# Optimization experiments

Hardware: AMD Instinct MI355X
Metric: run time of the kernel (lower is better)

Reference implementation:

```python
import jax, jax.numpy as jnp
import numpy as np

HID = 768        # config.hidden_size
MM_HID = 1024    # config.mmodal_hidden_size
N_Q = 64         # config.num_queries
WIN = 512        # config.window_size
LN_EPS = 1e-5


def _window_starts(m, n, w):
    # mirrors split_tensor's start-index logic (static, computed in numpy)
    step = max(1, (m - w) // (n - 1))
    starts = []
    for i in range(n):
        s = i * step
        if s + w > m:
            s = m - w
        starts.append(s)
    return np.asarray(starts, dtype=np.int32)


def layernorm(x, g, b):
    mu = jnp.mean(x, axis=-1, keepdims=True)
    var = jnp.var(x, axis=-1, keepdims=True)
    return (x - mu) * jax.lax.rsqrt(var + LN_EPS) * g + b


def setup_inputs() -> dict:
    key = jax.random.key(0)
    ks = jax.random.split(key, 12)
    b, m, li = 4, 8192, 77
    s = lambda fan_in: 1.0 / np.sqrt(fan_in)
    inp = {
        'x_mmodal': jax.random.normal(ks[0], (b, m, MM_HID), jnp.float32),
        'inst_feats': jax.random.normal(ks[1], (b, li, HID), jnp.float32),
        'queries': jax.random.normal(ks[2], (1, N_Q, HID), jnp.float32),
        'W_proj': jax.random.normal(ks[3], (HID, HID), jnp.float32) * s(HID),
        'b_proj': jnp.zeros((HID,), jnp.float32),
        'W_kv_inst': jax.random.normal(ks[4], (HID, 2 * HID), jnp.float32) * s(HID),
        'b_kv_inst': jnp.zeros((2 * HID,), jnp.float32),
        'W_out_inst': jax.random.normal(ks[5], (HID, HID), jnp.float32) * s(HID),
        'b_out_inst': jnp.zeros((HID,), jnp.float32),
        'W_kv_mm': jax.random.normal(ks[6], (MM_HID, 2 * HID), jnp.float32) * s(MM_HID),
        'b_kv_mm': jnp.zeros((2 * HID,), jnp.float32),
        'W_out_mm': jax.random.normal(ks[7], (HID, HID), jnp.float32) * s(HID),
        'b_out_mm': jnp.zeros((HID,), jnp.float32),
        'ln_g': jnp.ones((HID,), jnp.float32),
        'ln_b': jnp.zeros((HID,), jnp.float32),
    }
    return inp


def reference(x_mmodal, inst_feats, queries, W_proj, b_proj, W_kv_inst,
              b_kv_inst, W_out_inst, b_out_inst, W_kv_mm, b_kv_mm,
              W_out_mm, b_out_mm, ln_g, ln_b):
    b = x_mmodal.shape[0]
    scale = 1.0 / jnp.sqrt(jnp.asarray(HID, x_mmodal.dtype))

    # ---- dense cross-attention over instruction features ----
    inst = inst_feats @ W_proj + b_proj                      # (b, li, d)
    k, v = jnp.split(inst @ W_kv_inst + b_kv_inst, 2, axis=-1)
    k = layernorm(k, ln_g, ln_b)
    v = layernorm(v, ln_g, ln_b)
    q = jnp.broadcast_to(queries, (b, N_Q, HID))
    attn = jnp.einsum('bnd,bmd->bnm', q, k) * scale
    attn = jax.nn.softmax(attn, axis=-1)
    q = jnp.einsum('bnm,bmd->bnd', attn, v)
    q = layernorm(q @ W_out_inst + b_out_inst, ln_g, ln_b)

    # ---- swin-style overlapping windowed cross-attention over mmodal ----
    k, v = jnp.split(x_mmodal @ W_kv_mm + b_kv_mm, 2, axis=-1)
    k = layernorm(k, ln_g, ln_b)
    v = layernorm(v, ln_g, ln_b)
    m = k.shape[1]
    starts = _window_starts(m, N_Q, WIN)                     # (n,)
    idx = jnp.asarray(starts[:, None] + np.arange(WIN))      # (n, w)
    kw = k[:, idx]                                           # (b, n, w, d)
    vw = v[:, idx]                                           # (b, n, w, d)
    a = jnp.einsum('bnd,bnwd->bnw', q, kw) * scale
    a = jax.nn.softmax(a, axis=-1)
    out = jnp.einsum('bnw,bnwd->bnd', a, vw)
    out = layernorm(out @ W_out_mm + b_out_mm, ln_g, ln_b)
    return out
```

## Files before the change

### kernel.cpp

```cpp
#include <hip/hip_runtime.h>

#define HIDDEN 768
#define NQ 64
#define WINSZ 512
#define MSEQ 8192
#define BATCH 4
#define LI 77
#define MMHID 1024
#define LN_EPS 1e-5f
#define SCALE_QK 0.03608439182435161f

typedef __attribute__((ext_vector_type(8))) short short8v;
typedef __attribute__((ext_vector_type(4))) float f32x4;
typedef __attribute__((ext_vector_type(8))) unsigned short u16x8;

#define AS1 __attribute__((address_space(1)))
#define AS3 __attribute__((address_space(3)))

__device__ inline unsigned short f2bf(float f) {
    unsigned u = __float_as_uint(f);
    u += 0x7fffu + ((u >> 16) & 1u);
    return (unsigned short)(u >> 16);
}
__device__ inline float bf2f(unsigned short h) {
    return __uint_as_float(((unsigned)h) << 16);
}

__device__ inline void block_reduce2_256(float& s1, float& s2, float* sm) {
    #pragma unroll
    for (int o = 32; o; o >>= 1) { s1 += __shfl_down(s1, o); s2 += __shfl_down(s2, o); }
    int lane = threadIdx.x & 63, w = threadIdx.x >> 6;
    __syncthreads();
    if (lane == 0) { sm[w] = s1; sm[4 + w] = s2; }
    __syncthreads();
    s1 = sm[0] + sm[1] + sm[2] + sm[3];
    s2 = sm[4] + sm[5] + sm[6] + sm[7];
}

__global__ __launch_bounds__(256) void cvt_kernel(const float* __restrict__ in,
                                                  unsigned short* __restrict__ out, int n8) {
    int i = blockIdx.x * 256 + threadIdx.x;
    if (i >= n8) return;
    const float4* p = (const float4*)(in + (size_t)i * 8);
    float4 a = p[0], b = p[1];
    u16x8 o;
    o[0] = f2bf(a.x); o[1] = f2bf(a.y); o[2] = f2bf(a.z); o[3] = f2bf(a.w);
    o[4] = f2bf(b.x); o[5] = f2bf(b.y); o[6] = f2bf(b.z); o[7] = f2bf(b.w);
    *(u16x8*)(out + (size_t)i * 8) = o;
}

__global__ __launch_bounds__(256) void cvt_pad_kernel(const float* __restrict__ in,
                                                      unsigned short* __restrict__ out,
                                                      int n8_valid, int n8_total) {
    int i = blockIdx.x * 256 + threadIdx.x;
    if (i >= n8_total) return;
    u16x8 o = {};
    if (i < n8_valid) {
        const float4* p = (const float4*)(in + (size_t)i * 8);
        float4 a = p[0], b = p[1];
        o[0] = f2bf(a.x); o[1] = f2bf(a.y); o[2] = f2bf(a.z); o[3] = f2bf(a.w);
        o[4] = f2bf(b.x); o[5] = f2bf(b.y); o[6] = f2bf(b.z); o[7] = f2bf(b.w);
    }
    *(u16x8*)(out + (size_t)i * 8) = o;
}

__global__ __launch_bounds__(256) void cvt_q_pad_kernel(const float* __restrict__ q2,
                                                        unsigned short* __restrict__ q2bf) {
    int i = blockIdx.x * 256 + threadIdx.x;
    if (i >= BATCH * 128 * HIDDEN) return;
    int b = i / (128 * HIDDEN);
    int rem = i - b * 128 * HIDDEN;
    int r = rem / HIDDEN, d = rem - r * HIDDEN;
    float v = 0.f;
    if (r < 64) v = q2[((size_t)(b * 64 + r)) * HIDDEN + d] * SCALE_QK;
    q2bf[i] = f2bf(v);
}

__global__ __launch_bounds__(256) void transW_kernel(const float* __restrict__ W,
                                                     unsigned short* __restrict__ Wt,
                                                     int D, int C) {
    __shared__ float tile[32][33];
    int n0 = blockIdx.x * 32, k0 = blockIdx.y * 32;
    int tx = threadIdx.x, ty = threadIdx.y;
    #pragma unroll
    for (int i = 0; i < 32; i += 8)
        tile[ty + i][tx] = W[(size_t)(k0 + ty + i) * C + n0 + tx];
    __syncthreads();
    #pragma unroll
    for (int i = 0; i < 32; i += 8)
        Wt[(size_t)(n0 + ty + i) * D + k0 + tx] = f2bf(tile[tx][ty + i]);
}

#define GM 32768
#define GN 1536
#define GK 1024

__global__ __launch_bounds__(256) void gemm_kv_kernel(const unsigned short* __restrict__ A,
                                                      const unsigned short* __restrict__ Bt,
                                                      const float* __restrict__ bias,
                                                      unsigned short* __restrict__ C) {
    __shared__ unsigned short sA[128 * 64];
    __shared__ unsigned short sB[128 * 64];

    int nwg = gridDim.x;
    int bid = blockIdx.x;
    int wg = bid;
    if ((nwg & 7) == 0) { int cpx = nwg >> 3; wg = (bid & 7) * cpx + (bid >> 3); }
    int bm = wg / (GN / 128), bn = wg % (GN / 128);
    int row0 = bm * 128, col0 = bn * 128;

    int tid = threadIdx.x;
    int lane = tid & 63, wid = tid >> 6;
    int wr = wid >> 1, wc = wid & 1;

    f32x4 acc[4][4] = {};

    int rS[4], cS[4];
    #pragma unroll
    for (int i = 0; i < 4; i++) {
        int ch = wid * 4 + i;
        int r = ch * 8 + (lane >> 3);
        rS[i] = r;
        cS[i] = ((lane & 7) ^ (r & 7)) << 3;
    }

    for (int k0 = 0; k0 < GK; k0 += 64) {
        #pragma unroll
        for (int i = 0; i < 4; i++) {
            int ch = wid * 4 + i;
            const unsigned short* ga = A + (size_t)(row0 + rS[i]) * GK + k0 + cS[i];
            __builtin_amdgcn_global_load_lds((const AS1 unsigned int*)ga,
                                             (AS3 unsigned int*)&sA[ch * 512], 16, 0, 0);
            const unsigned short* gb = Bt + (size_t)(col0 + rS[i]) * GK + k0 + cS[i];
            __builtin_amdgcn_global_load_lds((const AS1 unsigned int*)gb,
                                             (AS3 unsigned int*)&sB[ch * 512], 16, 0, 0);
        }
        __syncthreads();

        #pragma unroll
        for (int kk = 0; kk < 64; kk += 32) {
            int ko = (kk + ((lane >> 4) << 3)) * 2;
            short8v af[4], bf[4];
            #pragma unroll
            for (int m = 0; m < 4; m++) {
                int r = wr * 64 + m * 16 + (lane & 15);
                int addr = r * 128 + (ko ^ ((r & 7) << 4));
                af[m] = *(const short8v*)((const char*)sA + addr);
            }
            #pragma unroll
            for (int n = 0; n < 4; n++) {
                int r = wc * 64 + n * 16 + (lane & 15);
                int addr = r * 128 + (ko ^ ((r & 7) << 4));
                bf[n] = *(const short8v*)((const char*)sB + addr);
            }
            #pragma unroll
            for (int m = 0; m < 4; m++)
                #pragma unroll
                for (int n = 0; n < 4; n++)
                    acc[m][n] = __builtin_amdgcn_mfma_f32_16x16x32_bf16(af[m], bf[n], acc[m][n], 0, 0, 0);
        }
        __syncthreads();
    }

    int crow = (lane >> 4) * 4;
    int ccol = lane & 15;
    #pragma unroll
    for (int m = 0; m < 4; m++) {
        #pragma unroll
        for (int n = 0; n < 4; n++) {
            int gc = col0 + wc * 64 + n * 16 + ccol;
            float bv = bias[gc];
            #pragma unroll
            for (int j = 0; j < 4; j++) {
                int gr = row0 + wr * 64 + m * 16 + crow + j;
                C[(size_t)gr * GN + gc] = f2bf(acc[m][n][j] + bv);
            }
        }
    }
}

template <int TK, bool OUT_BF16>
__global__ __launch_bounds__(256) void gemm_tile_kernel(const unsigned short* __restrict__ A,
                                                        const unsigned short* __restrict__ Bt,
                                                        const float* __restrict__ bias,
                                                        void* __restrict__ Cout, int N) {
    __shared__ unsigned short sA[128 * 64];
    __shared__ unsigned short sB[128 * 64];

    int row0 = blockIdx.x * 128, col0 = blockIdx.y * 128;
    int tid = threadIdx.x;
    int lane = tid & 63, wid = tid >> 6;
    int wr = wid >> 1, wc = wid & 1;

    f32x4 acc[4][4] = {};

    int rS[4], cS[4];
    #pragma unroll
    for (int i = 0; i < 4; i++) {
        int ch = wid * 4 + i;
        int r = ch * 8 + (lane >> 3);
        rS[i] = r;
        cS[i] = ((lane & 7) ^ (r & 7)) << 3;
    }

    for (int k0 = 0; k0 < TK; k0 += 64) {
        #pragma unroll
        for (int i = 0; i < 4; i++) {
            int ch = wid * 4 + i;
            const unsigned short* ga = A + (size_t)(row0 + rS[i]) * TK + k0 + cS[i];
            __builtin_amdgcn_global_load_lds((const AS1 unsigned int*)ga,
                                             (AS3 unsigned int*)&sA[ch * 512], 16, 0, 0);
            const unsigned short* gb = Bt + (size_t)(col0 + rS[i]) * TK + k0 + cS[i];
            __builtin_amdgcn_global_load_lds((const AS1 unsigned int*)gb,
                                             (AS3 unsigned int*)&sB[ch * 512], 16, 0, 0);
        }
        __syncthreads();

        #pragma unroll
        for (int kk = 0; kk < 64; kk += 32) {
            int ko = (kk + ((lane >> 4) << 3)) * 2;
            short8v af[4], bf[4];
            #pragma unroll
            for (int m = 0; m < 4; m++) {
                int r = wr * 64 + m * 16 + (lane & 15);
                int addr = r * 128 + (ko ^ ((r & 7) << 4));
                af[m] = *(const short8v*)((const char*)sA + addr);
            }
            #pragma unroll
            for (int n = 0; n < 4; n++) {
                int r = wc * 64 + n * 16 + (lane & 15);
                int addr = r * 128 + (ko ^ ((r & 7) << 4));
                bf[n] = *(const short8v*)((const char*)sB + addr);
            }
            #pragma unroll
            for (int m = 0; m < 4; m++)
                #pragma unroll
                for (int n = 0; n < 4; n++)
                    acc[m][n] = __builtin_amdgcn_mfma_f32_16x16x32_bf16(af[m], bf[n], acc[m][n], 0, 0, 0);
        }
        __syncthreads();
    }

    int crow = (lane >> 4) * 4;
    int ccol = lane & 15;
    #pragma unroll
    for (int m = 0; m < 4; m++) {
        #pragma unroll
        for (int n = 0; n < 4; n++) {
            int gc = col0 + wc * 64 + n * 16 + ccol;
            float bv = bias[gc];
            #pragma unroll
            for (int j = 0; j < 4; j++) {
                int gr = row0 + wr * 64 + m * 16 + crow + j;
                float v = acc[m][n][j] + bv;
                if (OUT_BF16) ((unsigned short*)Cout)[(size_t)gr * N + gc] = f2bf(v);
                else          ((float*)Cout)[(size_t)gr * N + gc] = v;
            }
        }
    }
}

__global__ __launch_bounds__(256) void gemm_scores_kernel(const unsigned short* __restrict__ Aall,
                                                          const unsigned short* __restrict__ kv,
                                                          float* __restrict__ scores) {
    __shared__ unsigned short sA[128 * 64];
    __shared__ unsigned short sB[128 * 64];

    int b = blockIdx.y;
    int col0 = blockIdx.x * 128;
    const unsigned short* A = Aall + (size_t)b * 128 * HIDDEN;
    const unsigned short* Bt = kv + (size_t)b * MSEQ * 1536;

    int tid = threadIdx.x;
    int lane = tid & 63, wid = tid >> 6;
    int wr = wid >> 1, wc = wid & 1;

    f32x4 acc[4][4] = {};

    int rS[4], cS[4];
    #pragma unroll
    for (int i = 0; i < 4; i++) {
        int ch = wid * 4 + i;
        int r = ch * 8 + (lane >> 3);
        rS[i] = r;
        cS[i] = ((lane & 7) ^ (r & 7)) << 3;
    }

    for (int k0 = 0; k0 < HIDDEN; k0 += 64) {
        #pragma unroll
        for (int i = 0; i < 4; i++) {
            int ch = wid * 4 + i;
            const unsigned short* ga = A + (size_t)rS[i] * HIDDEN + k0 + cS[i];
            __builtin_amdgcn_global_load_lds((const AS1 unsigned int*)ga,
                                             (AS3 unsigned int*)&sA[ch * 512], 16, 0, 0);
            const unsigned short* gb = Bt + (size_t)(col0 + rS[i]) * 1536 + k0 + cS[i];
            __builtin_amdgcn_global_load_lds((const AS1 unsigned int*)gb,
                                             (AS3 unsigned int*)&sB[ch * 512], 16, 0, 0);
        }
        __syncthreads();

        #pragma unroll
        for (int kk = 0; kk < 64; kk += 32) {
            int ko = (kk + ((lane >> 4) << 3)) * 2;
            short8v af[4], bf[4];
            #pragma unroll
            for (int m = 0; m < 4; m++) {
                int r = wr * 64 + m * 16 + (lane & 15);
                int addr = r * 128 + (ko ^ ((r & 7) << 4));
                af[m] = *(const short8v*)((const char*)sA + addr);
            }
            #pragma unroll
            for (int n = 0; n < 4; n++) {
                int r = wc * 64 + n * 16 + (lane & 15);
                int addr = r * 128 + (ko ^ ((r & 7) << 4));
                bf[n] = *(const short8v*)((const char*)sB + addr);
            }
            #pragma unroll
            for (int m = 0; m < 4; m++)
                #pragma unroll
                for (int n = 0; n < 4; n++)
                    acc[m][n] = __builtin_amdgcn_mfma_f32_16x16x32_bf16(af[m], bf[n], acc[m][n], 0, 0, 0);
        }
        __syncthreads();
    }

    int crow = (lane >> 4) * 4;
    int ccol = lane & 15;
    #pragma unroll
    for (int m = 0; m < 4; m++) {
        #pragma unroll
        for (int n = 0; n < 4; n++) {
            int gc = col0 + wc * 64 + n * 16 + ccol;
            #pragma unroll
            for (int j = 0; j < 4; j++) {
                int gr = wr * 64 + m * 16 + crow + j;
                if (gr < 64)
                    scores[((size_t)(b * 64 + gr)) * MSEQ + gc] = acc[m][n][j];
            }
        }
    }
}

__global__ __launch_bounds__(512) void win_softmax_kernel(const float* __restrict__ scores,
                                                          unsigned short* __restrict__ P_abs) {
    int bidx = blockIdx.x;
    int b = bidx >> 6, n = bidx & 63;
    int step = (MSEQ - WINSZ) / (NQ - 1);
    int s = n * step;
    if (s + WINSZ > MSEQ) s = MSEQ - WINSZ;

    __shared__ float sm[8];
    int t = threadIdx.x, lane = t & 63, w = t >> 6;
    const float* srow = scores + ((size_t)(b * 64 + n)) * MSEQ;
    float a = srow[s + t];

    float m = a;
    #pragma unroll
    for (int o = 32; o; o >>= 1) m = fmaxf(m, __shfl_down(m, o));
    if (lane == 0) sm[w] = m;
    __syncthreads();
    m = sm[0];
    #pragma unroll
    for (int i = 1; i < 8; i++) m = fmaxf(m, sm[i]);
    float e = expf(a - m);
    float ssum = e;
    #pragma unroll
    for (int o = 32; o; o >>= 1) ssum += __shfl_down(ssum, o);
    __syncthreads();
    if (lane == 0) sm[w] = ssum;
    __syncthreads();
    ssum = 0;
    #pragma unroll
    for (int i = 0; i < 8; i++) ssum += sm[i];

    unsigned short* prow = P_abs + ((size_t)(b * 64 + n)) * MSEQ;
    for (int pos = t; pos < MSEQ; pos += 512)
        if (pos < s || pos >= s + WINSZ) prow[pos] = 0;
    prow[s + t] = f2bf(e / ssum);
}

__global__ __launch_bounds__(768) void pv_chunk_kernel(const unsigned short* __restrict__ P_abs,
                                                       const unsigned short* __restrict__ kv,
                                                       float* __restrict__ out_acc) {
    int b = blockIdx.y;
    int r0 = blockIdx.x * 64;
    int t = threadIdx.x;

    int n_lo = (r0 >= 512) ? ((r0 - 512) / 121 + 1) : 0;
    int n_hi = (r0 + 63) / 121;
    if (n_hi > 63) n_hi = 63;

    __shared__ float pw[5][64];
    if (t < 5 * 64) {
        int ni = t >> 6, r = t & 63;
        int n = n_lo + ni;
        float v = 0.f;
        if (n <= n_hi)
            v = bf2f(P_abs[((size_t)(b * 64 + n)) * MSEQ + r0 + r]);
        pw[ni][r] = v;
    }
    __syncthreads();

    const unsigned short* vbase = kv + ((size_t)(b * MSEQ + r0)) * 1536 + 768;
    float acc[5] = {};
    #pragma unroll 8
    for (int r = 0; r < 64; ++r) {
        float v = bf2f(vbase[(size_t)r * 1536 + t]);
        #pragma unroll
        for (int ni = 0; ni < 5; ni++) acc[ni] = fmaf(v, pw[ni][r], acc[ni]);
    }
    #pragma unroll
    for (int ni = 0; ni < 5; ni++) {
        int n = n_lo + ni;
        if (n <= n_hi)
            atomicAdd(&out_acc[((size_t)(b * 64 + n)) * HIDDEN + t], acc[ni]);
    }
}

__global__ __launch_bounds__(256) void ln_bf16_kernel(unsigned short* __restrict__ kv,
                                                      const float* __restrict__ g,
                                                      const float* __restrict__ b) {
    int rh = blockIdx.x;
    unsigned short* p = kv + (size_t)rh * 768;
    int t = threadIdx.x;
    float x0 = bf2f(p[t]), x1 = bf2f(p[t + 256]), x2 = bf2f(p[t + 512]);
    float s = x0 + x1 + x2, s2 = x0 * x0 + x1 * x1 + x2 * x2;
    __shared__ float sm[8];
    block_reduce2_256(s, s2, sm);
    float mu = s * (1.f / 768.f);
    float var = s2 * (1.f / 768.f) - mu * mu;
    float inv = rsqrtf(var + LN_EPS);
    p[t]       = f2bf((x0 - mu) * inv * g[t]       + b[t]);
    p[t + 256] = f2bf((x1 - mu) * inv * g[t + 256] + b[t + 256]);
    p[t + 512] = f2bf((x2 - mu) * inv * g[t + 512] + b[t + 512]);
}

__global__ __launch_bounds__(256) void ln_f32_rows(float* __restrict__ base,
                                                   const float* __restrict__ g,
                                                   const float* __restrict__ b) {
    int rh = blockIdx.x;
    float* p = base + (size_t)rh * 768;
    int t = threadIdx.x;
    float x0 = p[t], x1 = p[t + 256], x2 = p[t + 512];
    float s = x0 + x1 + x2, s2 = x0 * x0 + x1 * x1 + x2 * x2;
    __shared__ float sm[8];
    block_reduce2_256(s, s2, sm);
    float mu = s * (1.f / 768.f);
    float var = s2 * (1.f / 768.f) - mu * mu;
    float inv = rsqrtf(var + LN_EPS);
    p[t]       = (x0 - mu) * inv * g[t]       + b[t];
    p[t + 256] = (x1 - mu) * inv * g[t + 256] + b[t + 256];
    p[t + 512] = (x2 - mu) * inv * g[t + 512] + b[t + 512];
}

__global__ __launch_bounds__(256) void attn_inst_kernel(const float* __restrict__ queries,
                                                        const float* __restrict__ kv,
                                                        unsigned short* __restrict__ qatt) {
    int bidx = blockIdx.x;
    int b = bidx >> 6, n = bidx & 63;
    __shared__ float qs[HIDDEN];
    __shared__ float sc[LI], sc2[LI];
    int t = threadIdx.x, lane = t & 63, w = t >> 6;
    const float* q = queries + (size_t)n * HIDDEN;
    for (int d = t; d < HIDDEN; d += 256) qs[d] = q[d];
    __syncthreads();
    const float* kb = kv + (size_t)b * LI * 1536;
    for (int j = w; j < LI; j += 4) {
        const float* kr = kb + (size_t)j * 1536;
        float a = 0;
        #pragma unroll
        for (int i = 0; i < 12; i++) { int d = lane + i * 64; a = fmaf(kr[d], qs[d], a); }
        #pragma unroll
        for (int o = 32; o; o >>= 1) a += __shfl_down(a, o);
        if (lane == 0) sc[j] = a * SCALE_QK;
    }
    __syncthreads();
    float m = -1e30f;
    for (int j = 0; j < LI; j++) m = fmaxf(m, sc[j]);
    if (t < LI) sc2[t] = expf(sc[t] - m);
    __syncthreads();
    float s = 0;
    for (int j = 0; j < LI; j++) s += sc2[j];
    float inv = 1.f / s;
    float o0 = 0, o1 = 0, o2 = 0;
    for (int j = 0; j < LI; j++) {
        float p = sc2[j] * inv;
        const float* vr = kb + (size_t)j * 1536 + 768;
        o0 = fmaf(p, vr[t], o0);
        o1 = fmaf(p, vr[t + 256], o1);
        o2 = fmaf(p, vr[t + 512], o2);
    }
    unsigned short* orow = qatt + ((size_t)b * NQ + n) * HIDDEN;
    orow[t] = f2bf(o0); orow[t + 256] = f2bf(o1); orow[t + 512] = f2bf(o2);
}

extern "C" void kernel_launch(void* const* d_in, const int* in_sizes, int n_in,
                              void* d_out, int out_size, void* d_ws, size_t ws_size,
                              hipStream_t stream) {
    (void)in_sizes; (void)n_in; (void)out_size; (void)ws_size;
    const float* x_mm    = (const float*)d_in[0];
    const float* instf   = (const float*)d_in[1];
    const float* queries = (const float*)d_in[2];
    const float* W_proj  = (const float*)d_in[3];
    const float* b_proj  = (const float*)d_in[4];
    const float* W_kvi   = (const float*)d_in[5];
    const float* b_kvi   = (const float*)d_in[6];
    const float* W_oi    = (const float*)d_in[7];
    const float* b_oi    = (const float*)d_in[8];
    const float* W_kvm   = (const float*)d_in[9];
    const float* b_kvm   = (const float*)d_in[10];
    const float* W_om    = (const float*)d_in[11];
    const float* b_om    = (const float*)d_in[12];
    const float* ln_g    = (const float*)d_in[13];
    const float* ln_b    = (const float*)d_in[14];
    float* out = (float*)d_out;

    char* ws = (char*)d_ws;
    size_t off = 0;
    auto carve = [&](size_t bytes) -> char* {
        char* p = ws + off;
        off += (bytes + 255) & ~(size_t)255;
        return p;
    };
    unsigned short* x_bf   = (unsigned short*)carve((size_t)BATCH * MSEQ * MMHID * 2);
    unsigned short* wtm_bf = (unsigned short*)carve((size_t)2 * HIDDEN * MMHID * 2);
    unsigned short* kv_mm  = (unsigned short*)carve((size_t)BATCH * MSEQ * 2 * HIDDEN * 2);
    unsigned short* wp_bf  = (unsigned short*)carve((size_t)768 * 768 * 2);
    unsigned short* wkvi_bf= (unsigned short*)carve((size_t)1536 * 768 * 2);
    unsigned short* woi_bf = (unsigned short*)carve((size_t)768 * 768 * 2);
    unsigned short* wom_bf = (unsigned short*)carve((size_t)768 * 768 * 2);
    unsigned short* a1_bf  = (unsigned short*)carve((size_t)384 * 768 * 2);
    unsigned short* inst_bf= (unsigned short*)carve((size_t)384 * 768 * 2);
    float*          kv_inst= (float*)carve((size_t)384 * 1536 * 4);
    unsigned short* qatt_bf= (unsigned short*)carve((size_t)256 * 768 * 2);
    float*          q2     = (float*)carve((size_t)256 * 768 * 4);
    unsigned short* q2bf   = (unsigned short*)carve((size_t)BATCH * 128 * 768 * 2);
    float*          scores = (float*)carve((size_t)BATCH * 64 * MSEQ * 4);
    unsigned short* P_abs  = (unsigned short*)carve((size_t)BATCH * 64 * MSEQ * 2);
    float*          o_acc  = (float*)carve((size_t)BATCH * 64 * 768 * 4);
    unsigned short* a_bf   = (unsigned short*)carve((size_t)256 * 768 * 2);

    transW_kernel<<<dim3(1536 / 32, 1024 / 32), dim3(32, 8), 0, stream>>>(W_kvm, wtm_bf, 1024, 1536);
    transW_kernel<<<dim3(768 / 32, 768 / 32), dim3(32, 8), 0, stream>>>(W_proj, wp_bf, 768, 768);
    transW_kernel<<<dim3(1536 / 32, 768 / 32), dim3(32, 8), 0, stream>>>(W_kvi, wkvi_bf, 768, 1536);
    transW_kernel<<<dim3(768 / 32, 768 / 32), dim3(32, 8), 0, stream>>>(W_oi, woi_bf, 768, 768);
    transW_kernel<<<dim3(768 / 32, 768 / 32), dim3(32, 8), 0, stream>>>(W_om, wom_bf, 768, 768);

    int n8 = BATCH * MSEQ * MMHID / 8;
    cvt_kernel<<<(n8 + 255) / 256, 256, 0, stream>>>(x_mm, x_bf, n8);
    gemm_kv_kernel<<<(GM / 128) * (GN / 128), 256, 0, stream>>>(x_bf, wtm_bf, b_kvm, kv_mm);
    ln_bf16_kernel<<<BATCH * MSEQ * 2, 256, 0, stream>>>(kv_mm, ln_g, ln_b);

    cvt_pad_kernel<<<(384 * 768 / 8 + 255) / 256, 256, 0, stream>>>(instf, a1_bf,
                                                                    BATCH * LI * 768 / 8, 384 * 768 / 8);
    gemm_tile_kernel<768, true><<<dim3(3, 6), 256, 0, stream>>>(a1_bf, wp_bf, b_proj, inst_bf, 768);
    gemm_tile_kernel<768, false><<<dim3(3, 12), 256, 0, stream>>>(inst_bf, wkvi_bf, b_kvi, kv_inst, 1536);
    ln_f32_rows<<<BATCH * LI * 2, 256, 0, stream>>>(kv_inst, ln_g, ln_b);
    attn_inst_kernel<<<BATCH * NQ, 256, 0, stream>>>(queries, kv_inst, qatt_bf);
    gemm_tile_kernel<768, false><<<dim3(2, 6), 256, 0, stream>>>(qatt_bf, woi_bf, b_oi, q2, 768);
    ln_f32_rows<<<BATCH * NQ, 256, 0, stream>>>(q2, ln_g, ln_b);

    hipMemsetAsync(o_acc, 0, (size_t)BATCH * 64 * 768 * 4, stream);
    cvt_q_pad_kernel<<<(BATCH * 128 * 768 + 255) / 256, 256, 0, stream>>>(q2, q2bf);
    gemm_scores_kernel<<<dim3(MSEQ / 128, BATCH), 256, 0, stream>>>(q2bf, kv_mm, scores);
    win_softmax_kernel<<<BATCH * NQ, 512, 0, stream>>>(scores, P_abs);
    pv_chunk_kernel<<<dim3(MSEQ / 64, BATCH), 768, 0, stream>>>(P_abs, kv_mm, o_acc);
    cvt_kernel<<<(256 * 768 / 8 + 255) / 256, 256, 0, stream>>>(o_acc, a_bf, 256 * 768 / 8);

    gemm_tile_kernel<768, false><<<dim3(2, 6), 256, 0, stream>>>(a_bf, wom_bf, b_om, out, 768);
    ln_f32_rows<<<BATCH * NQ, 256, 0, stream>>>(out, ln_g, ln_b);
}
```

Before: 367.6 us.

## Fold mmodal K/V layernorm into scores and output instead of rewriting KV

The in-place layernorm pass over the large bf16 KV buffer is replaced by a read-only stats kernel that stores per-row mu*inv and inv. The normalization is folded in algebraically in three places. The query is pre-scaled by gamma, and the scores are corrected with inv and a mean term built from the sum of the scaled query. The probabilities are scaled by the V-row inv, and the output applies gamma and beta after subtracting a weighted mean term. This removes a full write of the KV buffer. Separately, the five weight-transpose launches are merged into one batched launch. The cost is extra small kernels and reductions, plus some numerical sensitivity from working on un-normalized bf16 values.

Result: faster. 350.2 us (-4.7%).

```diff
diff --git a/kernel.cpp b/kernel.cpp
--- a/kernel.cpp
+++ b/kernel.cpp
@@ -64,24 +64,44 @@
     *(u16x8*)(out + (size_t)i * 8) = o;
 }
 
-__global__ __launch_bounds__(256) void cvt_q_pad_kernel(const float* __restrict__ q2,
-                                                        unsigned short* __restrict__ q2bf) {
-    int i = blockIdx.x * 256 + threadIdx.x;
-    if (i >= BATCH * 128 * HIDDEN) return;
-    int b = i / (128 * HIDDEN);
-    int rem = i - b * 128 * HIDDEN;
-    int r = rem / HIDDEN, d = rem - r * HIDDEN;
-    float v = 0.f;
-    if (r < 64) v = q2[((size_t)(b * 64 + r)) * HIDDEN + d] * SCALE_QK;
-    q2bf[i] = f2bf(v);
-}
-
-__global__ __launch_bounds__(256) void transW_kernel(const float* __restrict__ W,
-                                                     unsigned short* __restrict__ Wt,
-                                                     int D, int C) {
+__global__ __launch_bounds__(256) void cvt_q_kernel(const float* __restrict__ q2,
+                                                    const float* __restrict__ g,
+                                                    unsigned short* __restrict__ q2bf,
+                                                    float* __restrict__ qgsum) {
+    int blk = blockIdx.x;
+    int b = blk >> 7, r = blk & 127;
+    int t = threadIdx.x;
+    unsigned short* orow = q2bf + (size_t)blk * HIDDEN;
+    if (r >= 64) {
+        orow[t] = 0; orow[t + 256] = 0; orow[t + 512] = 0;
+        return;
+    }
+    const float* qrow = q2 + ((size_t)(b * 64 + r)) * HIDDEN;
+    float v0 = qrow[t]       * g[t]       * SCALE_QK;
+    float v1 = qrow[t + 256] * g[t + 256] * SCALE_QK;
+    float v2 = qrow[t + 512] * g[t + 512] * SCALE_QK;
+    orow[t] = f2bf(v0); orow[t + 256] = f2bf(v1); orow[t + 512] = f2bf(v2);
+    float s = v0 + v1 + v2, s2 = 0.f;
+    __shared__ float sm[8];
+    block_reduce2_256(s, s2, sm);
+    if (t == 0) qgsum[b * 64 + r] = s;
+}
+
+struct TWJobs {
+    const float* W[5];
+    unsigned short* Wt[5];
+    int D[5];
+    int C[5];
+};
+__global__ __launch_bounds__(256) void transW_all_kernel(TWJobs tw) {
+    int z = blockIdx.z;
+    int C = tw.C[z], D = tw.D[z];
+    int n0 = blockIdx.x * 32, k0 = blockIdx.y * 32;
+    if (n0 >= C || k0 >= D) return;
+    const float* W = tw.W[z];
+    unsigned short* Wt = tw.Wt[z];
     __shared__ float tile[32][33];
-    int n0 = blockIdx.x * 32, k0 = blockIdx.y * 32;
-    int tx = threadIdx.x, ty = threadIdx.y;
+    int tx = threadIdx.x & 31, ty = (threadIdx.x >> 5);
     #pragma unroll
     for (int i = 0; i < 32; i += 8)
         tile[ty + i][tx] = W[(size_t)(k0 + ty + i) * C + n0 + tx];
@@ -179,6 +199,23 @@
     }
 }
 
+__global__ __launch_bounds__(256) void stats_kernel(const unsigned short* __restrict__ kv,
+                                                    float2* __restrict__ stats) {
+    int rh = blockIdx.x;
+    const unsigned short* p = kv + (size_t)rh * 768;
+    int t = threadIdx.x;
+    float x0 = bf2f(p[t]), x1 = bf2f(p[t + 256]), x2 = bf2f(p[t + 512]);
+    float s = x0 + x1 + x2, s2 = x0 * x0 + x1 * x1 + x2 * x2;
+    __shared__ float sm[8];
+    block_reduce2_256(s, s2, sm);
+    if (t == 0) {
+        float mu = s * (1.f / 768.f);
+        float var = s2 * (1.f / 768.f) - mu * mu;
+        float inv = rsqrtf(var + LN_EPS);
+        stats[rh] = make_float2(mu * inv, inv);
+    }
+}
+
 template <int TK, bool OUT_BF16>
 __global__ __launch_bounds__(256) void gemm_tile_kernel(const unsigned short* __restrict__ A,
                                                         const unsigned short* __restrict__ Bt,
@@ -342,7 +379,10 @@
 }
 
 __global__ __launch_bounds__(512) void win_softmax_kernel(const float* __restrict__ scores,
-                                                          unsigned short* __restrict__ P_abs) {
+                                                          const float2* __restrict__ stats,
+                                                          const float* __restrict__ qgsum,
+                                                          unsigned short* __restrict__ P_abs,
+                                                          float* __restrict__ s2out) {
     int bidx = blockIdx.x;
     int b = bidx >> 6, n = bidx & 63;
     int step = (MSEQ - WINSZ) / (NQ - 1);
@@ -351,8 +391,11 @@
 
     __shared__ float sm[8];
     int t = threadIdx.x, lane = t & 63, w = t >> 6;
-    const float* srow = scores + ((size_t)(b * 64 + n)) * MSEQ;
-    float a = srow[s + t];
+    int r_abs = s + t;
+    size_t rowidx = (size_t)b * MSEQ + r_abs;
+    float2 stk = stats[rowidx * 2 + 0];
+    float qg = qgsum[b * 64 + n];
+    float a = stk.y * scores[((size_t)(b * 64 + n)) * MSEQ + r_abs] - qg * stk.x;
 
     float m = a;
     #pragma unroll
@@ -372,11 +415,27 @@
     ssum = 0;
     #pragma unroll
     for (int i = 0; i < 8; i++) ssum += sm[i];
+    float p = e / ssum;
+
+    float2 stv = stats[rowidx * 2 + 1];
+    float pt = p * stv.y;
+    float s2p = p * stv.x;
+    #pragma unroll
+    for (int o = 32; o; o >>= 1) s2p += __shfl_down(s2p, o);
+    __syncthreads();
+    if (lane == 0) sm[w] = s2p;
+    __syncthreads();
+    if (t == 0) {
+        float s2 = 0;
+        #pragma unroll
+        for (int i = 0; i < 8; i++) s2 += sm[i];
+        s2out[b * 64 + n] = s2;
+    }
 
     unsigned short* prow = P_abs + ((size_t)(b * 64 + n)) * MSEQ;
     for (int pos = t; pos < MSEQ; pos += 512)
         if (pos < s || pos >= s + WINSZ) prow[pos] = 0;
-    prow[s + t] = f2bf(e / ssum);
+    prow[r_abs] = f2bf(pt);
 }
 
 __global__ __launch_bounds__(768) void pv_chunk_kernel(const unsigned short* __restrict__ P_abs,
@@ -417,22 +476,15 @@
     }
 }
 
-__global__ __launch_bounds__(256) void ln_bf16_kernel(unsigned short* __restrict__ kv,
-                                                      const float* __restrict__ g,
-                                                      const float* __restrict__ b) {
-    int rh = blockIdx.x;
-    unsigned short* p = kv + (size_t)rh * 768;
-    int t = threadIdx.x;
-    float x0 = bf2f(p[t]), x1 = bf2f(p[t + 256]), x2 = bf2f(p[t + 512]);
-    float s = x0 + x1 + x2, s2 = x0 * x0 + x1 * x1 + x2 * x2;
-    __shared__ float sm[8];
-    block_reduce2_256(s, s2, sm);
-    float mu = s * (1.f / 768.f);
-    float var = s2 * (1.f / 768.f) - mu * mu;
-    float inv = rsqrtf(var + LN_EPS);
-    p[t]       = f2bf((x0 - mu) * inv * g[t]       + b[t]);
-    p[t + 256] = f2bf((x1 - mu) * inv * g[t + 256] + b[t + 256]);
-    p[t + 512] = f2bf((x2 - mu) * inv * g[t + 512] + b[t + 512]);
+__global__ __launch_bounds__(256) void out_affine_kernel(const float* __restrict__ o_acc,
+                                                         const float* __restrict__ s2,
+                                                         const float* __restrict__ g,
+                                                         const float* __restrict__ bb,
+                                                         unsigned short* __restrict__ a_bf) {
+    int i = blockIdx.x * 256 + threadIdx.x;
+    if (i >= BATCH * NQ * HIDDEN) return;
+    int n = i / HIDDEN, d = i - n * HIDDEN;
+    a_bf[i] = f2bf(g[d] * (o_acc[i] - s2[n]) + bb[d]);
 }
 
 __global__ __launch_bounds__(256) void ln_f32_rows(float* __restrict__ base,
@@ -539,17 +591,22 @@
     unsigned short* P_abs  = (unsigned short*)carve((size_t)BATCH * 64 * MSEQ * 2);
     float*          o_acc  = (float*)carve((size_t)BATCH * 64 * 768 * 4);
     unsigned short* a_bf   = (unsigned short*)carve((size_t)256 * 768 * 2);
-
-    transW_kernel<<<dim3(1536 / 32, 1024 / 32), dim3(32, 8), 0, stream>>>(W_kvm, wtm_bf, 1024, 1536);
-    transW_kernel<<<dim3(768 / 32, 768 / 32), dim3(32, 8), 0, stream>>>(W_proj, wp_bf, 768, 768);
-    transW_kernel<<<dim3(1536 / 32, 768 / 32), dim3(32, 8), 0, stream>>>(W_kvi, wkvi_bf, 768, 1536);
-    transW_kernel<<<dim3(768 / 32, 768 / 32), dim3(32, 8), 0, stream>>>(W_oi, woi_bf, 768, 768);
-    transW_kernel<<<dim3(768 / 32, 768 / 32), dim3(32, 8), 0, stream>>>(W_om, wom_bf, 768, 768);
+    float2*         stats  = (float2*)carve((size_t)BATCH * MSEQ * 2 * sizeof(float2));
+    float*          qgsum  = (float*)carve((size_t)256 * 4);
+    float*          s2     = (float*)carve((size_t)256 * 4);
+
+    TWJobs tw;
+    tw.W[0] = W_kvm;  tw.Wt[0] = wtm_bf;  tw.D[0] = 1024; tw.C[0] = 1536;
+    tw.W[1] = W_proj; tw.Wt[1] = wp_bf;   tw.D[1] = 768;  tw.C[1] = 768;
+    tw.W[2] = W_kvi;  tw.Wt[2] = wkvi_bf; tw.D[2] = 768;  tw.C[2] = 1536;
+    tw.W[3] = W_oi;   tw.Wt[3] = woi_bf;  tw.D[3] = 768;  tw.C[3] = 768;
+    tw.W[4] = W_om;   tw.Wt[4] = wom_bf;  tw.D[4] = 768;  tw.C[4] = 768;
+    transW_all_kernel<<<dim3(48, 32, 5), 256, 0, stream>>>(tw);
 
     int n8 = BATCH * MSEQ * MMHID / 8;
     cvt_kernel<<<(n8 + 255) / 256, 256, 0, stream>>>(x_mm, x_bf, n8);
     gemm_kv_kernel<<<(GM / 128) * (GN / 128), 256, 0, stream>>>(x_bf, wtm_bf, b_kvm, kv_mm);
-    ln_bf16_kernel<<<BATCH * MSEQ * 2, 256, 0, stream>>>(kv_mm, ln_g, ln_b);
+    stats_kernel<<<BATCH * MSEQ * 2, 256, 0, stream>>>(kv_mm, stats);
 
     cvt_pad_kernel<<<(384 * 768 / 8 + 255) / 256, 256, 0, stream>>>(instf, a1_bf,
                                                                     BATCH * LI * 768 / 8, 384 * 768 / 8);
@@ -561,11 +618,11 @@
     ln_f32_rows<<<BATCH * NQ, 256, 0, stream>>>(q2, ln_g, ln_b);
 
     hipMemsetAsync(o_acc, 0, (size_t)BATCH * 64 * 768 * 4, stream);
-    cvt_q_pad_kernel<<<(BATCH * 128 * 768 + 255) / 256, 256, 0, stream>>>(q2, q2bf);
+    cvt_q_kernel<<<BATCH * 128, 256, 0, stream>>>(q2, ln_g, q2bf, qgsum);
     gemm_scores_kernel<<<dim3(MSEQ / 128, BATCH), 256, 0, stream>>>(q2bf, kv_mm, scores);
-    win_softmax_kernel<<<BATCH * NQ, 512, 0, stream>>>(scores, P_abs);
+    win_softmax_kernel<<<BATCH * NQ, 512, 0, stream>>>(scores, stats, qgsum, P_abs, s2);
     pv_chunk_kernel<<<dim3(MSEQ / 64, BATCH), 768, 0, stream>>>(P_abs, kv_mm, o_acc);
-    cvt_kernel<<<(256 * 768 / 8 + 255) / 256, 256, 0, stream>>>(o_acc, a_bf, 256 * 768 / 8);
+    out_affine_kernel<<<(BATCH * NQ * HIDDEN + 255) / 256, 256, 0, stream>>>(o_acc, s2, ln_g, ln_b, a_bf);
 
     gemm_tile_kernel<768, false><<<dim3(2, 6), 256, 0, stream>>>(a_bf, wom_bf, b_om, out, 768);
     ln_f32_rows<<<BATCH * NQ, 256, 0, stream>>>(out, ln_g, ln_b);
```
